# Performance work log

Hardware: AMD Instinct MI355X
Metric: run time of the kernel (lower is better)

The kernel has to match this reference:

```python
import jax, jax.numpy as jnp
import numpy as np

RES = (256, 256)
FLOW_TEMP_REG = 1e-3
LOSS_SCALING = True
EPS = 1e-9


def get_interpolation(events, flow, tref, res):
    # events: [B,N,4] (ts,y,x,p); flow: [B,N,2] per-event (flow_y, flow_x)
    warped = events[:, :, 1:3] + (tref - events[:, :, 0:1]) * flow  # [B,N,2] (y,x)
    top_y = jnp.floor(warped[:, :, 0:1])
    bot_y = top_y + 1.0
    left_x = jnp.floor(warped[:, :, 1:2])
    right_x = left_x + 1.0
    # four bilinear corners stacked along the event dim -> [B,4N,2]
    idx = jnp.concatenate([
        jnp.concatenate([top_y, left_x], axis=2),
        jnp.concatenate([top_y, right_x], axis=2),
        jnp.concatenate([bot_y, left_x], axis=2),
        jnp.concatenate([bot_y, right_x], axis=2)], axis=1)
    w = jnp.maximum(0.0, 1.0 - jnp.abs(jnp.tile(warped, (1, 4, 1)) - idx))  # [B,4N,2]
    mask = ((idx[:, :, 0:1] >= 0) & (idx[:, :, 0:1] < res[0]) &
            (idx[:, :, 1:2] >= 0) & (idx[:, :, 1:2] < res[1])).astype(w.dtype)
    idx = idx * mask  # out-of-bounds -> pixel 0 with zero weight
    w = w * mask
    flat_idx = (idx[:, :, 0] * res[1] + idx[:, :, 1]).astype(jnp.int32)  # [B,4N]
    weights = w[:, :, 0] * w[:, :, 1]  # bilinear weight, [B,4N]
    return flat_idx, weights


def interpolate(flat_idx, w, npix):
    # per-batch scatter-add of weights into a flat pixel grid -> [B, H*W]
    return jax.vmap(lambda i, v: jax.ops.segment_sum(v, i, num_segments=npix))(flat_idx, w)


def scale_loss(iwe_pos, iwe_neg, iwe_pos_ts, iwe_neg_ts):
    loss = jnp.sum(iwe_pos_ts ** 2, axis=1) + jnp.sum(iwe_neg_ts ** 2, axis=1)  # [B]
    if LOSS_SCALING:
        nonzero_px = jnp.sum(((iwe_pos + iwe_neg) != 0).astype(loss.dtype), axis=1)
        loss = loss / (nonzero_px + EPS)
    return jnp.sum(loss)


def forward(event_list, flow, pol_mask, vector_list, max_ts):
    res = RES
    npix = res[0] * res[1]
    mt = jnp.asarray(max_ts, jnp.float32)
    pm = jnp.tile(pol_mask, (1, 4, 1))                    # [B,4N,2]
    ts4 = jnp.tile(event_list[:, :, 0], (1, 4))           # [B,4N]
    loss = jnp.float32(0.0)
    # forward warp (tref=max_ts, weight ts) and backward warp (tref=0, weight max_ts-ts)
    for tref, ts_w in ((mt, ts4), (jnp.float32(0.0), mt - ts4)):
        idx, w = get_interpolation(event_list, flow, tref, res)
        wp = w * pm[:, :, 0]
        wn = w * pm[:, :, 1]
        iwe_pos = interpolate(idx, wp, npix)
        iwe_neg = interpolate(idx, wn, npix)
        iwe_pos_ts = interpolate(idx, wp * ts_w, npix) / (iwe_pos + EPS) / mt
        iwe_neg_ts = interpolate(idx, wn * ts_w, npix) / (iwe_neg + EPS) / mt
        loss = loss + scale_loss(iwe_pos, iwe_neg, iwe_pos_ts, iwe_neg_ts)
    # single flow scale in _flow_list -> divide by 1
    loss = loss / 1.0
    # Charbonnier temporal smoothness on flow vectors [B,P,8]
    dt = vector_list[:, :-1, :] - vector_list[:, 1:, :]
    dt = jnp.sqrt(dt ** 2 + EPS).reshape(vector_list.shape[0], -1)
    loss = loss + FLOW_TEMP_REG * jnp.sum(jnp.mean(dt, axis=1))
    return loss


def setup_inputs() -> dict:
    B, N, P = 8, 262144, 4
    H, W = RES
    key = jax.random.key(0)
    ks = jax.random.split(key, 6)
    ts = jax.random.uniform(ks[0], (B, N, 1), dtype=jnp.float32) * P
    y = jax.random.uniform(ks[1], (B, N, 1), dtype=jnp.float32) * (H - 1)
    x = jax.random.uniform(ks[2], (B, N, 1), dtype=jnp.float32) * (W - 1)
    p = jax.random.bernoulli(ks[3], 0.5, (B, N, 1)).astype(jnp.float32) * 2.0 - 1.0
    event_list = jnp.concatenate([ts, y, x, p], axis=2)
    pos = (p > 0).astype(jnp.float32)
    pol_mask = jnp.concatenate([pos, 1.0 - pos], axis=2)
    flow = jax.random.normal(ks[4], (B, N, 2), dtype=jnp.float32) * 2.0
    vector_list = jax.random.normal(ks[5], (B, P, 8), dtype=jnp.float32)
    return {"event_list": event_list, "flow": flow, "pol_mask": pol_mask,
            "vector_list": vector_list, "max_ts": P}


def reference(event_list, flow, pol_mask, vector_list, max_ts):
    return forward(event_list, flow, pol_mask, vector_list, max_ts)
```

## Files before the change

kernel.cpp:

```cpp
#include <hip/hip_runtime.h>
#include <math.h>

#define RES_H 256
#define RES_W 256
#define NPIX 65536
#define EPSF 1e-9f
#define FLOW_TEMP_REG 1e-3f

#define BAND_SHIFT 4
#define BAND_ROWS 16
#define N_BANDS 16
#define BAND_PX (BAND_ROWS * RES_W)
#define CAP 24576
#define QS 2048.0f
#define QINV (1.0f / 2048.0f)
#define EV_PER_BLOCK 2048
#define EV_PER_THREAD 8

#define PAD 32

typedef unsigned long long u64;
typedef unsigned int u32;

__device__ __forceinline__ float decode_mt(const int* p) {
    int raw = *p;
    if (raw >= 0 && raw < (1 << 23)) return (float)raw;
    union { int i; float f; } u; u.i = raw; return u.f;
}


__global__ void __launch_bounds__(256) ew_bin(
    const float4* __restrict__ ev, const float2* __restrict__ flow,
    const int* __restrict__ mt_ptr, u64* __restrict__ recs,
    u32* __restrict__ counts, int N)
{
    __shared__ u32 hist[32], basebuf[32], cursor[32];
    const int b = blockIdx.y;
    const int start = blockIdx.x * EV_PER_BLOCK;
    const int tid = threadIdx.x;
    if (tid < 32) { hist[tid] = 0u; cursor[tid] = 0u; }
    __syncthreads();

    const float mt = decode_mt(mt_ptr);
    const float inv_mt = 1.0f / mt;

    float4 e[EV_PER_THREAD];
    float2 f[EV_PER_THREAD];
    #pragma unroll
    for (int j = 0; j < EV_PER_THREAD; ++j) {
        int i = start + tid + j * 256;
        if (i < N) { e[j] = ev[b * N + i]; f[j] = flow[b * N + i]; }
        else { e[j] = make_float4(0.f, -100.f, -100.f, 1.f); f[j] = make_float2(0.f, 0.f); }
    }

    #pragma unroll
    for (int j = 0; j < EV_PER_THREAD; ++j) {
        #pragma unroll
        for (int dir = 0; dir < 2; ++dir) {
            float dtt = (dir ? 0.0f : mt) - e[j].x;
            float wy = fminf(fmaxf(e[j].y + dtt * f[j].x, -8.0f), 264.0f);
            float wx = fminf(fmaxf(e[j].z + dtt * f[j].y, -8.0f), 264.0f);
            int wyf = __float2int_rn(wy * 4096.0f);
            int wxf = __float2int_rn(wx * 4096.0f);
            int iy = wyf >> 12, ix = wxf >> 12;
            if (iy < -1 || iy > 255 || ix < -1 || ix > 255) continue;
            int t1 = iy >> BAND_SHIFT;
            int t2 = (iy + 1) >> BAND_SHIFT;
            if (t1 >= 0) atomicAdd(&hist[dir * 16 + t1], 1u);
            if (t2 <= 15 && t2 != t1) atomicAdd(&hist[dir * 16 + t2], 1u);
        }
    }
    __syncthreads();
    if (tid < 32) basebuf[tid] = atomicAdd(&counts[(b * 32 + tid) * PAD], hist[tid]);
    __syncthreads();

    #pragma unroll
    for (int j = 0; j < EV_PER_THREAD; ++j) {
        #pragma unroll
        for (int dir = 0; dir < 2; ++dir) {
            float dtt = (dir ? 0.0f : mt) - e[j].x;
            float tswn = (dir ? (mt - e[j].x) : e[j].x) * inv_mt;
            float wy = fminf(fmaxf(e[j].y + dtt * f[j].x, -8.0f), 264.0f);
            float wx = fminf(fmaxf(e[j].z + dtt * f[j].y, -8.0f), 264.0f);
            int wyf = __float2int_rn(wy * 4096.0f);
            int wxf = __float2int_rn(wx * 4096.0f);
            int iy = wyf >> 12, ix = wxf >> 12;
            if (iy < -1 || iy > 255 || ix < -1 || ix > 255) continue;
            u32 tq = __float2uint_rn(fminf(fmaxf(tswn, 0.0f), 1.0f) * 4096.0f);
            u64 rec = (u64)((u32)wyf & 0x3FFFFFu)
                    | ((u64)((u32)wxf & 0x3FFFFFu) << 22)
                    | ((u64)tq << 44)
                    | ((u64)(e[j].w > 0.0f ? 0u : 1u) << 57);
            int t1 = iy >> BAND_SHIFT;
            int t2 = (iy + 1) >> BAND_SHIFT;
            #pragma unroll
            for (int s = 0; s < 2; ++s) {
                int t = s ? t2 : t1;
                if (t < 0 || t > 15) continue;
                if (s && t2 == t1) continue;
                int k = dir * 16 + t;
                u32 off = atomicAdd(&cursor[k], 1u);
                u32 slot = basebuf[k] + off;
                if (slot >= CAP) slot = CAP - 1;
                recs[(size_t)(b * 32 + k) * CAP + slot] = rec;
            }
        }
    }
}

__global__ void __launch_bounds__(1024) ew_accum(
    const u64* __restrict__ recs, const u32* __restrict__ counts,
    float* __restrict__ partials)
{
    __shared__ u32 lds[2 * BAND_PX];
    __shared__ float wterm[16], wnz[16];
    const int band = blockIdx.x, bd = blockIdx.y;
    const int q = bd * 16 + band;
    const int row0 = band << BAND_SHIFT;
    const int tid = threadIdx.x;
    for (int i = tid; i < 2 * BAND_PX; i += 1024) lds[i] = 0u;
    __syncthreads();

    u32 cnt = counts[q * PAD]; if (cnt > CAP) cnt = CAP;
    const u64* bucket = recs + (size_t)q * CAP;

    for (u32 i = tid; i < cnt; i += 1024) {
        u64 rec = bucket[i];
        int wyf = ((int)(((u32)rec & 0x3FFFFFu) << 10)) >> 10;
        int wxf = ((int)(((u32)(rec >> 22) & 0x3FFFFFu) << 10)) >> 10;
        float tswn = (float)((u32)(rec >> 44) & 0x1FFFu) * (1.0f / 4096.0f);
        u32 pol = (u32)(rec >> 57) & 1u;
        int ry = (wyf >> 12) - row0;
        int ix = wxf >> 12;
        float fy = (float)(wyf & 0xFFF) * (1.0f / 4096.0f);
        float fx = (float)(wxf & 0xFFF) * (1.0f / 4096.0f);
        u32* pl = lds + pol * BAND_PX;
        #pragma unroll
        for (int cc = 0; cc < 4; ++cc) {
            int cy = ry + (cc >> 1), cx = ix + (cc & 1);
            if ((unsigned)cy >= BAND_ROWS || (unsigned)cx >= RES_W) continue;
            float wgt = ((cc >> 1) ? fy : 1.0f - fy) * ((cc & 1) ? fx : 1.0f - fx);
            u32 v = (__float2uint_rn(wgt * tswn * QS) << 16)
                  |  __float2uint_rn(wgt * QS);
            if (v) atomicAdd(&pl[(cy << 8) | cx], v);
        }
    }
    __syncthreads();

    const uint4 pp = ((const uint4*)lds)[tid];
    const uint4 nn = ((const uint4*)(lds + BAND_PX))[tid];
    const u32 pu[4] = {pp.x, pp.y, pp.z, pp.w};
    const u32 nu[4] = {nn.x, nn.y, nn.z, nn.w};
    float term = 0.0f, nz = 0.0f;
    #pragma unroll
    for (int j = 0; j < 4; ++j) {
        u32 wp_r = pu[j] & 0xFFFFu, tp_r = pu[j] >> 16;
        u32 wn_r = nu[j] & 0xFFFFu, tn_r = nu[j] >> 16;
        float wp = (float)wp_r * QINV, tp = (float)tp_r * QINV;
        float wn = (float)wn_r * QINV, tn = (float)tn_r * QINV;
        float pts = tp / (wp + EPSF);
        float nts = tn / (wn + EPSF);
        term += pts * pts + nts * nts;
        nz   += ((wp_r | wn_r) != 0u) ? 1.0f : 0.0f;
    }
    #pragma unroll
    for (int off = 32; off > 0; off >>= 1) {
        term += __shfl_down(term, off);
        nz   += __shfl_down(nz, off);
    }
    if ((tid & 63) == 0) { wterm[tid >> 6] = term; wnz[tid >> 6] = nz; }
    __syncthreads();
    if (tid == 0) {
        float t = 0.0f, z = 0.0f;
        #pragma unroll
        for (int wv = 0; wv < 16; ++wv) { t += wterm[wv]; z += wnz[wv]; }
        atomicAdd(&partials[bd * PAD + 0], t);
        atomicAdd(&partials[bd * PAD + 1], z);
    }
}

__global__ void __launch_bounds__(256) ew_finalize(
    const float* __restrict__ partials, const float* __restrict__ vec,
    float* __restrict__ out, int B, int P, int n_bd)
{
    int tid = threadIdx.x;
    float v = 0.0f;
    if (tid < n_bd) {
        float s = partials[tid * PAD + 0];
        float n = partials[tid * PAD + 1];
        v = s / (n + EPSF);
    }
    int per_b = (P - 1) * 8;
    int total = B * per_b;
    float sm = 0.0f;
    for (int i = tid; i < total; i += blockDim.x) {
        int b = i / per_b;
        int r = i - b * per_b;
        int pi = r >> 3, j = r & 7;
        float d = vec[(b * P + pi) * 8 + j] - vec[(b * P + pi + 1) * 8 + j];
        sm += sqrtf(d * d + EPSF);
    }
    sm = sm / (float)per_b * FLOW_TEMP_REG;

    __shared__ float sdata[256];
    sdata[tid] = v + sm;
    __syncthreads();
    for (int s = 128; s > 0; s >>= 1) {
        if (tid < s) sdata[tid] += sdata[tid + s];
        __syncthreads();
    }
    if (tid == 0) out[0] = sdata[0];
}

extern "C" void kernel_launch(void* const* d_in, const int* in_sizes, int n_in,
                              void* d_out, int out_size, void* d_ws, size_t ws_size,
                              hipStream_t stream) {
    const float4* ev   = (const float4*)d_in[0];
    const float2* flow = (const float2*)d_in[1];
    const float*  vec  = (const float*)d_in[3];
    const int*    mtp  = (const int*)d_in[4];

    const int B = 8;
    const int N = in_sizes[0] / (B * 4);
    const int P = in_sizes[3] / (B * 8);

    u32*   counts   = (u32*)d_ws;
    float* partials = (float*)((char*)d_ws + 32768);
    u64*   recs     = (u64*)((char*)d_ws + 65536);

    hipMemsetAsync(d_ws, 0, 65536, stream);

    dim3 bgrid((N + EV_PER_BLOCK - 1) / EV_PER_BLOCK, B);
    ew_bin<<<bgrid, 256, 0, stream>>>(ev, flow, mtp, recs, counts, N);

    dim3 agrid(N_BANDS, 16);
    ew_accum<<<agrid, 1024, 0, stream>>>(recs, counts, partials);

    ew_finalize<<<1, 256, 0, stream>>>(partials, vec, (float*)d_out, B, P, 16);
}
```

Before: 127.1 us.

## Use per-block fixed-slot bins, drop histogram pass, memset and finalize kernel

Each binning block now writes its records into its own fixed 256-slot region per (batch, direction, band) and stores a per-block count. This removes the counting histogram pass and the global atomic offset reservation. The accumulate kernel walks all block slots and masks out the unused ones. The separate memset and finalize kernel are replaced by zeroing inside the bin kernel and a last-block-done reduction in the accumulate kernel, which saves launches but scans padded slots and truncates silently if a block overflows 256 records per bucket.

```diff
diff --git a/kernel.cpp b/kernel.cpp
--- a/kernel.cpp
+++ b/kernel.cpp
@@ -3,7 +3,6 @@
 
 #define RES_H 256
 #define RES_W 256
-#define NPIX 65536
 #define EPSF 1e-9f
 #define FLOW_TEMP_REG 1e-3f
 
@@ -11,12 +10,14 @@
 #define BAND_ROWS 16
 #define N_BANDS 16
 #define BAND_PX (BAND_ROWS * RES_W)
-#define CAP 24576
 #define QS 2048.0f
 #define QINV (1.0f / 2048.0f)
 #define EV_PER_BLOCK 2048
 #define EV_PER_THREAD 8
 
+#define CAP_BLK 256
+#define SLOT_SHIFT 8
+#define NBK_MAX 512
 #define PAD 32
 
 typedef unsigned long long u64;
@@ -29,16 +30,20 @@
 }
 
 
+
 __global__ void __launch_bounds__(256) ew_bin(
     const float4* __restrict__ ev, const float2* __restrict__ flow,
     const int* __restrict__ mt_ptr, u64* __restrict__ recs,
-    u32* __restrict__ counts, int N)
+    u32* __restrict__ scnt, float* __restrict__ pz, int N, int nbk)
 {
-    __shared__ u32 hist[32], basebuf[32], cursor[32];
-    const int b = blockIdx.y;
-    const int start = blockIdx.x * EV_PER_BLOCK;
+    __shared__ u32 cursor[32];
+    const int b  = blockIdx.y;
+    const int bk = blockIdx.x;
+    const int start = bk * EV_PER_BLOCK;
     const int tid = threadIdx.x;
-    if (tid < 32) { hist[tid] = 0u; cursor[tid] = 0u; }
+    if (tid < 32) cursor[tid] = 0u;
+    if (bk == 0 && b == 0)
+        for (int i = tid; i < 2048; i += 256) pz[i] = 0.0f;
     __syncthreads();
 
     const float mt = decode_mt(mt_ptr);
@@ -52,27 +57,6 @@
         if (i < N) { e[j] = ev[b * N + i]; f[j] = flow[b * N + i]; }
         else { e[j] = make_float4(0.f, -100.f, -100.f, 1.f); f[j] = make_float2(0.f, 0.f); }
     }
-
-    #pragma unroll
-    for (int j = 0; j < EV_PER_THREAD; ++j) {
-        #pragma unroll
-        for (int dir = 0; dir < 2; ++dir) {
-            float dtt = (dir ? 0.0f : mt) - e[j].x;
-            float wy = fminf(fmaxf(e[j].y + dtt * f[j].x, -8.0f), 264.0f);
-            float wx = fminf(fmaxf(e[j].z + dtt * f[j].y, -8.0f), 264.0f);
-            int wyf = __float2int_rn(wy * 4096.0f);
-            int wxf = __float2int_rn(wx * 4096.0f);
-            int iy = wyf >> 12, ix = wxf >> 12;
-            if (iy < -1 || iy > 255 || ix < -1 || ix > 255) continue;
-            int t1 = iy >> BAND_SHIFT;
-            int t2 = (iy + 1) >> BAND_SHIFT;
-            if (t1 >= 0) atomicAdd(&hist[dir * 16 + t1], 1u);
-            if (t2 <= 15 && t2 != t1) atomicAdd(&hist[dir * 16 + t2], 1u);
-        }
-    }
-    __syncthreads();
-    if (tid < 32) basebuf[tid] = atomicAdd(&counts[(b * 32 + tid) * PAD], hist[tid]);
-    __syncthreads();
 
     #pragma unroll
     for (int j = 0; j < EV_PER_THREAD; ++j) {
@@ -100,49 +84,59 @@
                 if (s && t2 == t1) continue;
                 int k = dir * 16 + t;
                 u32 off = atomicAdd(&cursor[k], 1u);
-                u32 slot = basebuf[k] + off;
-                if (slot >= CAP) slot = CAP - 1;
-                recs[(size_t)(b * 32 + k) * CAP + slot] = rec;
+                if (off >= CAP_BLK) off = CAP_BLK - 1;
+                recs[((size_t)((b * 32 + k) * nbk + bk) << SLOT_SHIFT) + off] = rec;
             }
         }
     }
+    __syncthreads();
+    if (tid < 32) {
+        u32 c = cursor[tid]; if (c > CAP_BLK) c = CAP_BLK;
+        scnt[(b * 32 + tid) * nbk + bk] = c;
+    }
 }
 
 __global__ void __launch_bounds__(1024) ew_accum(
-    const u64* __restrict__ recs, const u32* __restrict__ counts,
-    float* __restrict__ partials)
+    const u64* __restrict__ recs, const u32* __restrict__ scnt,
+    float* __restrict__ partials, const float* __restrict__ vec,
+    float* __restrict__ out, int nbk, int B, int P)
 {
     __shared__ u32 lds[2 * BAND_PX];
+    __shared__ u32 cnt[NBK_MAX];
     __shared__ float wterm[16], wnz[16];
+    __shared__ int is_last_s;
     const int band = blockIdx.x, bd = blockIdx.y;
-    const int q = bd * 16 + band;
+    const int b = bd >> 1, k = (bd & 1) * 16 + band;
     const int row0 = band << BAND_SHIFT;
     const int tid = threadIdx.x;
+
     for (int i = tid; i < 2 * BAND_PX; i += 1024) lds[i] = 0u;
-    __syncthreads();
-
-    u32 cnt = counts[q * PAD]; if (cnt > CAP) cnt = CAP;
-    const u64* bucket = recs + (size_t)q * CAP;
-
-    for (u32 i = tid; i < cnt; i += 1024) {
-        u64 rec = bucket[i];
-        int wyf = ((int)(((u32)rec & 0x3FFFFFu) << 10)) >> 10;
-        int wxf = ((int)(((u32)(rec >> 22) & 0x3FFFFFu) << 10)) >> 10;
-        float tswn = (float)((u32)(rec >> 44) & 0x1FFFu) * (1.0f / 4096.0f);
-        u32 pol = (u32)(rec >> 57) & 1u;
-        int ry = (wyf >> 12) - row0;
-        int ix = wxf >> 12;
-        float fy = (float)(wyf & 0xFFF) * (1.0f / 4096.0f);
-        float fx = (float)(wxf & 0xFFF) * (1.0f / 4096.0f);
-        u32* pl = lds + pol * BAND_PX;
-        #pragma unroll
-        for (int cc = 0; cc < 4; ++cc) {
-            int cy = ry + (cc >> 1), cx = ix + (cc & 1);
-            if ((unsigned)cy >= BAND_ROWS || (unsigned)cx >= RES_W) continue;
-            float wgt = ((cc >> 1) ? fy : 1.0f - fy) * ((cc & 1) ? fx : 1.0f - fx);
-            u32 v = (__float2uint_rn(wgt * tswn * QS) << 16)
-                  |  __float2uint_rn(wgt * QS);
-            if (v) atomicAdd(&pl[(cy << 8) | cx], v);
+    for (int i = tid; i < nbk; i += 1024) cnt[i] = scnt[(b * 32 + k) * nbk + i];
+    __syncthreads();
+
+    const u64* bucket = recs + ((size_t)((b * 32 + k) * nbk) << SLOT_SHIFT);
+    const int total = nbk << SLOT_SHIFT;
+    for (int g = tid; g < total; g += 1024) {
+        if ((u32)(g & (CAP_BLK - 1)) < cnt[g >> SLOT_SHIFT]) {
+            u64 rec = bucket[g];
+            int wyf = ((int)(((u32)rec & 0x3FFFFFu) << 10)) >> 10;
+            int wxf = ((int)(((u32)(rec >> 22) & 0x3FFFFFu) << 10)) >> 10;
+            float tswn = (float)((u32)(rec >> 44) & 0x1FFFu) * (1.0f / 4096.0f);
+            u32 pol = (u32)(rec >> 57) & 1u;
+            int ry = (wyf >> 12) - row0;
+            int ix = wxf >> 12;
+            float fy = (float)(wyf & 0xFFF) * (1.0f / 4096.0f);
+            float fx = (float)(wxf & 0xFFF) * (1.0f / 4096.0f);
+            u32* pl = lds + pol * BAND_PX;
+            #pragma unroll
+            for (int cc = 0; cc < 4; ++cc) {
+                int cy = ry + (cc >> 1), cx = ix + (cc & 1);
+                if ((unsigned)cy >= BAND_ROWS || (unsigned)cx >= RES_W) continue;
+                float wgt = ((cc >> 1) ? fy : 1.0f - fy) * ((cc & 1) ? fx : 1.0f - fx);
+                u32 v = (__float2uint_rn(wgt * tswn * QS) << 16)
+                      |  __float2uint_rn(wgt * QS);
+                if (v) atomicAdd(&pl[(cy << 8) | cx], v);
+            }
         }
     }
     __syncthreads();
@@ -170,46 +164,55 @@
     }
     if ((tid & 63) == 0) { wterm[tid >> 6] = term; wnz[tid >> 6] = nz; }
     __syncthreads();
+
+    u32* done  = (u32*)(partials + 512);
+    u32* done2 = (u32*)(partials + 1024);
     if (tid == 0) {
         float t = 0.0f, z = 0.0f;
         #pragma unroll
         for (int wv = 0; wv < 16; ++wv) { t += wterm[wv]; z += wnz[wv]; }
         atomicAdd(&partials[bd * PAD + 0], t);
         atomicAdd(&partials[bd * PAD + 1], z);
-    }
-}
-
-__global__ void __launch_bounds__(256) ew_finalize(
-    const float* __restrict__ partials, const float* __restrict__ vec,
-    float* __restrict__ out, int B, int P, int n_bd)
-{
-    int tid = threadIdx.x;
+        __threadfence();
+        int last = 0;
+        if (atomicAdd(&done[bd * PAD], 1u) == N_BANDS - 1u) {
+            if (atomicAdd(done2, 1u) == 15u) last = 1;
+        }
+        is_last_s = last;
+    }
+    __syncthreads();
+    if (!is_last_s) return;
+
+    __threadfence();
     float v = 0.0f;
-    if (tid < n_bd) {
-        float s = partials[tid * PAD + 0];
-        float n = partials[tid * PAD + 1];
+    if (tid < 16) {
+        float s = __hip_atomic_load(&partials[tid * PAD + 0],
+                                    __ATOMIC_RELAXED, __HIP_MEMORY_SCOPE_AGENT);
+        float n = __hip_atomic_load(&partials[tid * PAD + 1],
+                                    __ATOMIC_RELAXED, __HIP_MEMORY_SCOPE_AGENT);
         v = s / (n + EPSF);
     }
-    int per_b = (P - 1) * 8;
-    int total = B * per_b;
+    const int per_b = (P - 1) * 8;
+    const int tot = B * per_b;
     float sm = 0.0f;
-    for (int i = tid; i < total; i += blockDim.x) {
-        int b = i / per_b;
-        int r = i - b * per_b;
+    for (int i = tid; i < tot; i += 1024) {
+        int bb = i / per_b;
+        int r = i - bb * per_b;
         int pi = r >> 3, j = r & 7;
-        float d = vec[(b * P + pi) * 8 + j] - vec[(b * P + pi + 1) * 8 + j];
+        float d = vec[(bb * P + pi) * 8 + j] - vec[(bb * P + pi + 1) * 8 + j];
         sm += sqrtf(d * d + EPSF);
     }
-    sm = sm / (float)per_b * FLOW_TEMP_REG;
-
-    __shared__ float sdata[256];
-    sdata[tid] = v + sm;
-    __syncthreads();
-    for (int s = 128; s > 0; s >>= 1) {
-        if (tid < s) sdata[tid] += sdata[tid + s];
-        __syncthreads();
-    }
-    if (tid == 0) out[0] = sdata[0];
+    float val = v + sm / (float)per_b * FLOW_TEMP_REG;
+    #pragma unroll
+    for (int off = 32; off > 0; off >>= 1) val += __shfl_down(val, off);
+    if ((tid & 63) == 0) wterm[tid >> 6] = val;
+    __syncthreads();
+    if (tid == 0) {
+        float t = 0.0f;
+        #pragma unroll
+        for (int wv = 0; wv < 16; ++wv) t += wterm[wv];
+        out[0] = t;
+    }
 }
 
 extern "C" void kernel_launch(void* const* d_in, const int* in_sizes, int n_in,
@@ -223,18 +226,17 @@
     const int B = 8;
     const int N = in_sizes[0] / (B * 4);
     const int P = in_sizes[3] / (B * 8);
-
-    u32*   counts   = (u32*)d_ws;
-    float* partials = (float*)((char*)d_ws + 32768);
-    u64*   recs     = (u64*)((char*)d_ws + 65536);
-
-    hipMemsetAsync(d_ws, 0, 65536, stream);
-
-    dim3 bgrid((N + EV_PER_BLOCK - 1) / EV_PER_BLOCK, B);
-    ew_bin<<<bgrid, 256, 0, stream>>>(ev, flow, mtp, recs, counts, N);
+    int nbk = (N + EV_PER_BLOCK - 1) / EV_PER_BLOCK;
+    if (nbk > NBK_MAX) nbk = NBK_MAX;
+
+    float* partials = (float*)d_ws;
+    u32*   scnt     = (u32*)((char*)d_ws + 8192);
+    u64*   recs     = (u64*)((char*)d_ws + 524288);
+
+    dim3 bgrid(nbk, B);
+    ew_bin<<<bgrid, 256, 0, stream>>>(ev, flow, mtp, recs, scnt, partials, N, nbk);
 
     dim3 agrid(N_BANDS, 16);
-    ew_accum<<<agrid, 1024, 0, stream>>>(recs, counts, partials);
-
-    ew_finalize<<<1, 256, 0, stream>>>(partials, vec, (float*)d_out, B, P, 16);
-}
+    ew_accum<<<agrid, 1024, 0, stream>>>(recs, scnt, partials, vec,
+                                         (float*)d_out, nbk, B, P);
+}
```

Result: slower. 140.4 us (+10.5%).

## Cache packed records across binning passes and fuse finalize into accumulate kernel

Applied to the files above, without the earlier changes.

The binning kernel now builds each event's packed record once during the histogram pass and keeps it in registers, with a validity mask, instead of recomputing the warp in the scatter pass. The finalize kernel is removed; the last accumulate block to finish, found via global atomic counters, computes the final loss. This removes one launch and the duplicated arithmetic. The cost is higher register pressure from holding 16 u64 records per thread, plus a threadfence and atomic handshake.

```diff
diff --git a/kernel.cpp b/kernel.cpp
--- a/kernel.cpp
+++ b/kernel.cpp
@@ -3,7 +3,6 @@
 
 #define RES_H 256
 #define RES_W 256
-#define NPIX 65536
 #define EPSF 1e-9f
 #define FLOW_TEMP_REG 1e-3f
 
@@ -27,6 +26,7 @@
     if (raw >= 0 && raw < (1 << 23)) return (float)raw;
     union { int i; float f; } u; u.i = raw; return u.f;
 }
+
 
 
 __global__ void __launch_bounds__(256) ew_bin(
@@ -44,53 +44,47 @@
     const float mt = decode_mt(mt_ptr);
     const float inv_mt = 1.0f / mt;
 
-    float4 e[EV_PER_THREAD];
-    float2 f[EV_PER_THREAD];
+    u64 rc[EV_PER_THREAD][2];
+    u32 vm = 0u;
     #pragma unroll
     for (int j = 0; j < EV_PER_THREAD; ++j) {
         int i = start + tid + j * 256;
-        if (i < N) { e[j] = ev[b * N + i]; f[j] = flow[b * N + i]; }
-        else { e[j] = make_float4(0.f, -100.f, -100.f, 1.f); f[j] = make_float2(0.f, 0.f); }
-    }
-
-    #pragma unroll
-    for (int j = 0; j < EV_PER_THREAD; ++j) {
+        float4 e; float2 f;
+        if (i < N) { e = ev[b * N + i]; f = flow[b * N + i]; }
+        else { e = make_float4(0.f, -100.f, -100.f, 1.f); f = make_float2(0.f, 0.f); }
         #pragma unroll
         for (int dir = 0; dir < 2; ++dir) {
-            float dtt = (dir ? 0.0f : mt) - e[j].x;
-            float wy = fminf(fmaxf(e[j].y + dtt * f[j].x, -8.0f), 264.0f);
-            float wx = fminf(fmaxf(e[j].z + dtt * f[j].y, -8.0f), 264.0f);
-            int wyf = __float2int_rn(wy * 4096.0f);
-            int wxf = __float2int_rn(wx * 4096.0f);
-            int iy = wyf >> 12, ix = wxf >> 12;
-            if (iy < -1 || iy > 255 || ix < -1 || ix > 255) continue;
-            int t1 = iy >> BAND_SHIFT;
-            int t2 = (iy + 1) >> BAND_SHIFT;
-            if (t1 >= 0) atomicAdd(&hist[dir * 16 + t1], 1u);
-            if (t2 <= 15 && t2 != t1) atomicAdd(&hist[dir * 16 + t2], 1u);
-        }
-    }
-    __syncthreads();
-    if (tid < 32) basebuf[tid] = atomicAdd(&counts[(b * 32 + tid) * PAD], hist[tid]);
-    __syncthreads();
-
-    #pragma unroll
-    for (int j = 0; j < EV_PER_THREAD; ++j) {
-        #pragma unroll
-        for (int dir = 0; dir < 2; ++dir) {
-            float dtt = (dir ? 0.0f : mt) - e[j].x;
-            float tswn = (dir ? (mt - e[j].x) : e[j].x) * inv_mt;
-            float wy = fminf(fmaxf(e[j].y + dtt * f[j].x, -8.0f), 264.0f);
-            float wx = fminf(fmaxf(e[j].z + dtt * f[j].y, -8.0f), 264.0f);
+            float dtt = (dir ? 0.0f : mt) - e.x;
+            float tswn = (dir ? (mt - e.x) : e.x) * inv_mt;
+            float wy = fminf(fmaxf(e.y + dtt * f.x, -8.0f), 264.0f);
+            float wx = fminf(fmaxf(e.z + dtt * f.y, -8.0f), 264.0f);
             int wyf = __float2int_rn(wy * 4096.0f);
             int wxf = __float2int_rn(wx * 4096.0f);
             int iy = wyf >> 12, ix = wxf >> 12;
             if (iy < -1 || iy > 255 || ix < -1 || ix > 255) continue;
             u32 tq = __float2uint_rn(fminf(fmaxf(tswn, 0.0f), 1.0f) * 4096.0f);
-            u64 rec = (u64)((u32)wyf & 0x3FFFFFu)
-                    | ((u64)((u32)wxf & 0x3FFFFFu) << 22)
-                    | ((u64)tq << 44)
-                    | ((u64)(e[j].w > 0.0f ? 0u : 1u) << 57);
+            rc[j][dir] = (u64)((u32)wyf & 0x3FFFFFu)
+                       | ((u64)((u32)wxf & 0x3FFFFFu) << 22)
+                       | ((u64)tq << 44)
+                       | ((u64)(e.w > 0.0f ? 0u : 1u) << 57);
+            vm |= 1u << (j * 2 + dir);
+            int t1 = iy >> BAND_SHIFT;
+            int t2 = (iy + 1) >> BAND_SHIFT;
+            if (t1 >= 0) atomicAdd(&hist[dir * 16 + t1], 1u);
+            if (t2 <= 15 && t2 != t1) atomicAdd(&hist[dir * 16 + t2], 1u);
+        }
+    }
+    __syncthreads();
+    if (tid < 32) basebuf[tid] = atomicAdd(&counts[(b * 32 + tid) * PAD], hist[tid]);
+    __syncthreads();
+
+    #pragma unroll
+    for (int j = 0; j < EV_PER_THREAD; ++j) {
+        #pragma unroll
+        for (int dir = 0; dir < 2; ++dir) {
+            if (!(vm & (1u << (j * 2 + dir)))) continue;
+            u64 rec = rc[j][dir];
+            int iy = ((int)(((u32)rec & 0x3FFFFFu) << 10)) >> 22;
             int t1 = iy >> BAND_SHIFT;
             int t2 = (iy + 1) >> BAND_SHIFT;
             #pragma unroll
@@ -110,10 +104,12 @@
 
 __global__ void __launch_bounds__(1024) ew_accum(
     const u64* __restrict__ recs, const u32* __restrict__ counts,
-    float* __restrict__ partials)
+    float* __restrict__ partials, const float* __restrict__ vec,
+    float* __restrict__ out, int B, int P)
 {
     __shared__ u32 lds[2 * BAND_PX];
     __shared__ float wterm[16], wnz[16];
+    __shared__ int is_last_s;
     const int band = blockIdx.x, bd = blockIdx.y;
     const int q = bd * 16 + band;
     const int row0 = band << BAND_SHIFT;
@@ -170,46 +166,55 @@
     }
     if ((tid & 63) == 0) { wterm[tid >> 6] = term; wnz[tid >> 6] = nz; }
     __syncthreads();
+
+    u32* done  = (u32*)(partials + 512);
+    u32* done2 = (u32*)(partials + 1024);
     if (tid == 0) {
         float t = 0.0f, z = 0.0f;
         #pragma unroll
         for (int wv = 0; wv < 16; ++wv) { t += wterm[wv]; z += wnz[wv]; }
         atomicAdd(&partials[bd * PAD + 0], t);
         atomicAdd(&partials[bd * PAD + 1], z);
-    }
-}
-
-__global__ void __launch_bounds__(256) ew_finalize(
-    const float* __restrict__ partials, const float* __restrict__ vec,
-    float* __restrict__ out, int B, int P, int n_bd)
-{
-    int tid = threadIdx.x;
+        __threadfence();
+        int last = 0;
+        if (atomicAdd(&done[bd * PAD], 1u) == N_BANDS - 1u) {
+            if (atomicAdd(done2, 1u) == 15u) last = 1;
+        }
+        is_last_s = last;
+    }
+    __syncthreads();
+    if (!is_last_s) return;
+
+    __threadfence();
     float v = 0.0f;
-    if (tid < n_bd) {
-        float s = partials[tid * PAD + 0];
-        float n = partials[tid * PAD + 1];
+    if (tid < 16) {
+        float s = __hip_atomic_load(&partials[tid * PAD + 0],
+                                    __ATOMIC_RELAXED, __HIP_MEMORY_SCOPE_AGENT);
+        float n = __hip_atomic_load(&partials[tid * PAD + 1],
+                                    __ATOMIC_RELAXED, __HIP_MEMORY_SCOPE_AGENT);
         v = s / (n + EPSF);
     }
-    int per_b = (P - 1) * 8;
-    int total = B * per_b;
+    const int per_b = (P - 1) * 8;
+    const int tot = B * per_b;
     float sm = 0.0f;
-    for (int i = tid; i < total; i += blockDim.x) {
-        int b = i / per_b;
-        int r = i - b * per_b;
+    for (int i = tid; i < tot; i += 1024) {
+        int bb = i / per_b;
+        int r = i - bb * per_b;
         int pi = r >> 3, j = r & 7;
-        float d = vec[(b * P + pi) * 8 + j] - vec[(b * P + pi + 1) * 8 + j];
+        float d = vec[(bb * P + pi) * 8 + j] - vec[(bb * P + pi + 1) * 8 + j];
         sm += sqrtf(d * d + EPSF);
     }
-    sm = sm / (float)per_b * FLOW_TEMP_REG;
-
-    __shared__ float sdata[256];
-    sdata[tid] = v + sm;
-    __syncthreads();
-    for (int s = 128; s > 0; s >>= 1) {
-        if (tid < s) sdata[tid] += sdata[tid + s];
-        __syncthreads();
-    }
-    if (tid == 0) out[0] = sdata[0];
+    float val = v + sm / (float)per_b * FLOW_TEMP_REG;
+    #pragma unroll
+    for (int off = 32; off > 0; off >>= 1) val += __shfl_down(val, off);
+    if ((tid & 63) == 0) wterm[tid >> 6] = val;
+    __syncthreads();
+    if (tid == 0) {
+        float t = 0.0f;
+        #pragma unroll
+        for (int wv = 0; wv < 16; ++wv) t += wterm[wv];
+        out[0] = t;
+    }
 }
 
 extern "C" void kernel_launch(void* const* d_in, const int* in_sizes, int n_in,
@@ -224,8 +229,8 @@
     const int N = in_sizes[0] / (B * 4);
     const int P = in_sizes[3] / (B * 8);
 
+    float* partials = (float*)((char*)d_ws + 32768);
     u32*   counts   = (u32*)d_ws;
-    float* partials = (float*)((char*)d_ws + 32768);
     u64*   recs     = (u64*)((char*)d_ws + 65536);
 
     hipMemsetAsync(d_ws, 0, 65536, stream);
@@ -234,7 +239,6 @@
     ew_bin<<<bgrid, 256, 0, stream>>>(ev, flow, mtp, recs, counts, N);
 
     dim3 agrid(N_BANDS, 16);
-    ew_accum<<<agrid, 1024, 0, stream>>>(recs, counts, partials);
-
-    ew_finalize<<<1, 256, 0, stream>>>(partials, vec, (float*)d_out, B, P, 16);
-}
+    ew_accum<<<agrid, 1024, 0, stream>>>(recs, counts, partials, vec,
+                                         (float*)d_out, B, P);
+}
```

Result: slower. 132.6 us (+4.3%).
